# Performance work log

Measured on AMD Instinct MI355X. Metric: run time of the kernel, lower is better.

The kernel has to match this reference:

```python
import jax, jax.numpy as jnp
import numpy as np

B, S, TK, H, E, V, OOV = 16, 8, 400, 256, 128, 50000, 50
H2 = 2 * H


def setup_inputs() -> dict:
    key = jax.random.key(0)
    ks = jax.random.split(key, 24)
    std = 0.02
    d = {}
    d["y_t_1"] = jax.random.randint(ks[0], (B,), 0, V)
    d["h0"] = jax.random.normal(ks[1], (B, H), jnp.float32)
    d["c0"] = jax.random.normal(ks[2], (B, H), jnp.float32)
    d["encoder_output"] = jax.random.normal(ks[3], (B, S, TK, H2), jnp.float32)
    d["section_output"] = jax.random.normal(ks[4], (B, S, H2), jnp.float32)
    d["enc_padding_mask"] = jnp.ones((B, S, TK), jnp.float32)
    d["c_t_1"] = jax.random.normal(ks[5], (B, H2), jnp.float32)
    d["extra_zeros"] = jnp.zeros((B, OOV), jnp.float32)
    d["enc_batch_extend_vocab"] = jax.random.randint(ks[6], (B, S * TK), 0, V + OOV)
    d["coverage"] = jnp.zeros((B, S, TK), jnp.float32)
    d["gamma"] = jnp.ones((B, S, TK), jnp.float32)
    # learned parameters
    d["embedding"] = std * jax.random.normal(ks[7], (V, E), jnp.float32)
    d["W_xc"] = std * jax.random.normal(ks[8], (H2 + E, E), jnp.float32)
    d["b_xc"] = jnp.zeros((E,), jnp.float32)
    d["W_ih"] = std * jax.random.normal(ks[9], (E, 4 * H), jnp.float32)
    d["b_ih"] = jnp.zeros((4 * H,), jnp.float32)
    d["W_hh"] = std * jax.random.normal(ks[10], (H, 4 * H), jnp.float32)
    # pytorch init sets forget-gate bias (2nd quarter) to 1
    d["b_hh"] = jnp.zeros((4 * H,), jnp.float32).at[H:2 * H].set(1.0)
    d["Wh_sec"] = std * jax.random.normal(ks[11], (H2, H2), jnp.float32)
    d["Wd_sec"] = std * jax.random.normal(ks[12], (H2, H2), jnp.float32)
    d["bd_sec"] = jnp.zeros((H2,), jnp.float32)
    d["v_sec"] = std * jax.random.normal(ks[13], (H2, 1), jnp.float32)
    d["Wh_w"] = std * jax.random.normal(ks[14], (H2, H2), jnp.float32)
    d["Wc_w"] = std * jax.random.normal(ks[15], (H2,), jnp.float32)
    d["Wd_w"] = std * jax.random.normal(ks[16], (H2, H2), jnp.float32)
    d["bd_w"] = jnp.zeros((H2,), jnp.float32)
    d["v_w"] = std * jax.random.normal(ks[17], (H2, 1), jnp.float32)
    d["W_pgen"] = std * jax.random.normal(ks[18], (4 * H + E, 1), jnp.float32)
    d["b_pgen"] = jnp.zeros((1,), jnp.float32)
    d["W_out1"] = std * jax.random.normal(ks[19], (3 * H, H), jnp.float32)
    d["b_out1"] = jnp.zeros((H,), jnp.float32)
    d["W_out2"] = std * jax.random.normal(ks[20], (H, V), jnp.float32)
    d["b_out2"] = jnp.zeros((V,), jnp.float32)
    return d


def reference(y_t_1, h0, c0, encoder_output, section_output, enc_padding_mask,
              c_t_1, extra_zeros, enc_batch_extend_vocab, coverage, gamma,
              embedding, W_xc, b_xc, W_ih, b_ih, W_hh, b_hh,
              Wh_sec, Wd_sec, bd_sec, v_sec,
              Wh_w, Wc_w, Wd_w, bd_w, v_w,
              W_pgen, b_pgen, W_out1, b_out1, W_out2, b_out2):
    # embedding + input context projection
    emb = embedding[y_t_1]                                      # [B,E]
    x = jnp.concatenate([c_t_1, emb], axis=1) @ W_xc + b_xc     # [B,E]
    # single-step LSTM (pytorch gate order i,f,g,o)
    gates = x @ W_ih + b_ih + h0 @ W_hh + b_hh                  # [B,4H]
    i, f, g, o = jnp.split(gates, 4, axis=1)
    c = jax.nn.sigmoid(f) * c0 + jax.nn.sigmoid(i) * jnp.tanh(g)
    h = jax.nn.sigmoid(o) * jnp.tanh(c)
    s_t_hat = jnp.concatenate([h, c], axis=1)                   # [B,2H]
    # section attention -> beta [B,S]
    e_sec = jnp.tanh(section_output @ Wh_sec + (s_t_hat @ Wd_sec + bd_sec)[:, None, :])
    sc_sec = jnp.squeeze(e_sec @ v_sec, -1)                     # [B,S]
    beta = jax.nn.softmax(sc_sec, axis=1)
    beta = beta / beta.sum(axis=1, keepdims=True)
    # word attention with coverage feature
    att = encoder_output @ Wh_w + (s_t_hat @ Wd_w + bd_w)[:, None, None, :]
    att = att + coverage[..., None] * Wc_w                      # [B,S,TK,2H]
    sc_w = jnp.squeeze(jnp.tanh(att) @ v_w, -1)                 # [B,S,TK]
    ws = (beta[:, :, None] * sc_w).reshape(B, S * TK)
    mask = enc_padding_mask.reshape(B, S * TK)
    ad = jax.nn.softmax(ws, axis=1) * mask
    attn = ad / ad.sum(axis=1, keepdims=True)                   # [B,S*TK]
    c_t = jnp.einsum('bt,btn->bn', attn, encoder_output.reshape(B, S * TK, H2))
    cov = coverage + attn.reshape(B, S, TK)
    # pointer-gen gate
    p_gen = jax.nn.sigmoid(jnp.concatenate([c_t, s_t_hat, x], axis=1) @ W_pgen + b_pgen)  # [B,1]
    # output vocab distribution
    out = jnp.concatenate([h, c_t], axis=1) @ W_out1 + b_out1
    vocab_dist = jax.nn.softmax(out @ W_out2 + b_out2, axis=1)  # [B,V]
    vd = jnp.concatenate([p_gen * vocab_dist, extra_zeros], axis=1)  # [B,V+OOV]
    ad_ = (1.0 - p_gen) * attn
    rows = jnp.arange(B)[:, None]
    final_dist = vd.at[rows, enc_batch_extend_vocab].add(ad_)
    return (final_dist, h, c, c_t, attn, p_gen, cov)
```

## Files before the change

### kernel.cpp

```cpp
#include <hip/hip_runtime.h>
#include <math.h>

#define BB   16
#define SS   8
#define TKK  400
#define HH   256
#define EE   128
#define VV   50000
#define OOVV 50
#define HH2  512
#define STK  (SS*TKK)
#define VOO  (VV+OOVV)

#define OFF_X     0
#define OFF_ST    2048
#define OFF_SD    10240
#define OFF_WD    18432
#define OFF_SCSEC 26752
#define OFF_SCW   26880
#define OFF_CT    78080
#define OFF_OUT1  86272
#define OFF_PGEN  90368
#define OFF_PSUM  93520
#define OFF_BT    113040

#define O_FD   0
#define O_H    800800
#define O_C    804896
#define O_CT   808992
#define O_ATTN 817184
#define O_PGEN 868384
#define O_COV  868400

#define NLB 391
#define GEMM_NB 800

typedef __attribute__((ext_vector_type(8))) short bf16x8;
typedef __attribute__((ext_vector_type(4))) float f32x4;

__device__ __forceinline__ float sigm(float x){ return 1.0f/(1.0f+expf(-x)); }

__device__ __forceinline__ unsigned short f2b(float f){
  unsigned int u = __float_as_uint(f);
  unsigned int r = (u + 0x7fffu + ((u >> 16) & 1u)) >> 16;
  return (unsigned short)r;
}

__device__ __forceinline__ float tanhfast(float x){
  float cx = fminf(9.0f, fmaxf(-9.0f, x));
  float t = __expf(2.0f*cx);
  return (t - 1.0f) * __builtin_amdgcn_rcpf(t + 1.0f);
}

__device__ __forceinline__ float wave_sum(float v){
  #pragma unroll
  for(int o=32;o>0;o>>=1) v += __shfl_xor(v,o);
  return v;
}
__device__ __forceinline__ float wave_max(float v){
  #pragma unroll
  for(int o=32;o>0;o>>=1) v = fmaxf(v,__shfl_xor(v,o));
  return v;
}

__device__ __forceinline__ void glds16(const void* g, void* l){
  __builtin_amdgcn_global_load_lds((const __attribute__((address_space(1))) void*)g,
                                   (__attribute__((address_space(3))) void*)l, 16, 0, 0);
}

__device__ __forceinline__ bf16x8 cvt8(float4 a, float4 b){
  union{ bf16x8 v; unsigned short u[8]; } t;
  t.u[0]=f2b(a.x); t.u[1]=f2b(a.y); t.u[2]=f2b(a.z); t.u[3]=f2b(a.w);
  t.u[4]=f2b(b.x); t.u[5]=f2b(b.y); t.u[6]=f2b(b.z); t.u[7]=f2b(b.w);
  return t.v;
}

__global__ void k_pre(const float* __restrict__ Whw, unsigned short* __restrict__ Btg,
                      const int* __restrict__ y, const float* __restrict__ ct1,
                      const float* __restrict__ emb, const float* __restrict__ Wxc,
                      const float* __restrict__ bxc, const float* __restrict__ bdsec,
                      const float* __restrict__ bdw, float* __restrict__ ws){
  __shared__ float sm[10440];
  int bi = blockIdx.x, tid = threadIdx.x;
  if(bi < 64){
    int n0 = (bi & 7)*64, k0 = (bi >> 3)*64;
    int tx = tid & 63, ty = tid >> 6;
    #pragma unroll
    for(int it=0; it<16; it++){
      int kk = it*4 + ty;
      sm[kk*65 + tx] = Whw[(size_t)(k0+kk)*HH2 + n0 + tx];
    }
    __syncthreads();
    #pragma unroll
    for(int it=0; it<2; it++){
      int kgl = it*4 + ty;
      int kgG = (k0 >> 3) + kgl;
      int rnd = kgG >> 2, kg = kgG & 3;
      int col = n0 + tx;
      union{ bf16x8 v; unsigned short u[8]; } t;
      #pragma unroll
      for(int j=0;j<8;j++) t.u[j] = f2b(sm[(kgl*8+j)*65 + tx]);
      *(bf16x8*)&Btg[(size_t)rnd*16384 + (size_t)(col*4 + (kg ^ ((col>>1)&3)))*8] = t.v;
    }
  } else if(bi < 80){
    float* cat = sm;
    float* red = sm + 10240;
    for(int f=tid; f<BB*640; f+=256){
      int b = f/640, r = f - b*640;
      cat[f] = (r < HH2) ? ct1[b*HH2 + r] : emb[(size_t)y[b]*EE + (r-HH2)];
    }
    __syncthreads();
    int c = (bi-64)*8 + (tid & 7);
    int b = (tid >> 3) & 15;
    int kh = tid >> 7;
    float acc = 0.0f;
    const float* a = &cat[b*640];
    for(int k=kh*320; k<kh*320+320; k++) acc += a[k]*Wxc[k*EE + c];
    if(kh==1) red[b*8 + (tid&7)] = acc;
    __syncthreads();
    if(kh==0) ws[OFF_X + b*EE + c] = acc + red[b*8 + (tid&7)] + bxc[c];
  } else {
    for(int f=tid; f<BB*HH2; f+=256){
      int c = f & (HH2-1);
      ws[OFF_CT + f] = 0.0f;
      ws[OFF_SD + f] = bdsec[c];
      ws[OFF_WD + f] = bdw[c];
    }
  }
}

__global__ void k_lstm(const float* __restrict__ h0, const float* __restrict__ c0,
                       const float* __restrict__ Wih, const float* __restrict__ bih,
                       const float* __restrict__ Whh, const float* __restrict__ bhh,
                       float* __restrict__ ws, float* __restrict__ out){
  __shared__ float xh[4*384];
  __shared__ float red[3*64*4];
  int tid = threadIdx.x;
  int jc = (blockIdx.x & 15)*16, bc = (blockIdx.x >> 4)*4;
  for(int f=tid; f<4*384; f+=256){
    int bl = f/384, r = f - bl*384;
    xh[f] = (r < EE) ? ws[OFF_X + (bc+bl)*EE + r] : h0[(bc+bl)*HH + (r-EE)];
  }
  __syncthreads();
  int jl = tid & 15, bl = (tid >> 4) & 3, kq = tid >> 6;
  int j = jc + jl, b = bc + bl;
  float a0=0.f, a1=0.f, a2=0.f, a3=0.f;
  const float* a = &xh[bl*384];
  for(int k=kq*96; k<kq*96+96; k++){
    float v = a[k];
    const float* w = (k < EE) ? &Wih[k*4*HH + j] : &Whh[(k-EE)*4*HH + j];
    a0 += v*w[0]; a1 += v*w[HH]; a2 += v*w[2*HH]; a3 += v*w[3*HH];
  }
  if(kq){
    float* r = &red[((kq-1)*64 + bl*16 + jl)*4];
    r[0]=a0; r[1]=a1; r[2]=a2; r[3]=a3;
  }
  __syncthreads();
  if(kq==0){
    #pragma unroll
    for(int p=0;p<3;p++){
      const float* r = &red[(p*64 + bl*16 + jl)*4];
      a0+=r[0]; a1+=r[1]; a2+=r[2]; a3+=r[3];
    }
    a0 += bih[j] + bhh[j];
    a1 += bih[j+HH] + bhh[j+HH];
    a2 += bih[j+2*HH] + bhh[j+2*HH];
    a3 += bih[j+3*HH] + bhh[j+3*HH];
    float c = sigm(a1)*c0[b*HH+j] + sigm(a0)*tanhf(a2);
    float h = sigm(a3)*tanhf(c);
    out[O_H + b*HH + j] = h;
    out[O_C + b*HH + j] = c;
    ws[OFF_ST + b*HH2 + j]      = h;
    ws[OFF_ST + b*HH2 + HH + j] = c;
  }
}

__global__ void k_proj(const float* __restrict__ Wdsec, const float* __restrict__ Wdw,
                       float* __restrict__ ws){
  __shared__ float st[BB*32];
  int tid = threadIdx.x;
  int mi = blockIdx.x >> 5;
  int cb = (blockIdx.x >> 4) & 1;
  int kq = blockIdx.x & 15;
  int k0 = kq*32;
  for(int f=tid; f<BB*32; f+=256){
    int b = f >> 5, kk = f & 31;
    st[f] = ws[OFF_ST + b*HH2 + k0 + kk];
  }
  __syncthreads();
  int c = cb*256 + tid;
  const float* Wm = (mi ? Wdw : Wdsec) + (size_t)k0*HH2 + c;
  float acc[BB];
  #pragma unroll
  for(int b=0;b<BB;b++) acc[b] = 0.0f;
  #pragma unroll 4
  for(int kk=0;kk<32;kk++){
    float wv = Wm[(size_t)kk*HH2];
    #pragma unroll
    for(int b=0;b<BB;b++) acc[b] += st[b*32 + kk]*wv;
  }
  int dst = mi ? OFF_WD : OFF_SD;
  #pragma unroll
  for(int b=0;b<BB;b++) atomicAdd(&ws[dst + b*HH2 + c], acc[b]);
}

__global__ __launch_bounds__(512, 4) void k_gemm6(
        const float* __restrict__ A, const unsigned short* __restrict__ Btg,
        const float* __restrict__ Wcw, const float* __restrict__ vw,
        const float* __restrict__ cover,
        const float* __restrict__ sec, const float* __restrict__ Whsec,
        const float* __restrict__ vsec, float* __restrict__ ws){
  __shared__ __align__(16) unsigned short smem[32768];
  int tid = threadIdx.x;
  if(blockIdx.x >= GEMM_NB){
    float* row = (float*)smem;
    float* red = row + HH2;
    int bi = blockIdx.x - GEMM_NB;
    int b = bi >> 3;
    if(tid < HH2) row[tid] = sec[(size_t)bi*HH2 + tid];
    __syncthreads();
    int col = tid;
    float acc = 0.0f;
    #pragma unroll 8
    for(int k=0;k<HH2;k++) acc += row[k]*Whsec[k*HH2 + col];
    float val = tanhf(acc + ws[OFF_SD + b*HH2 + col]) * vsec[col];
    val = wave_sum(val);
    if((tid&63)==0) red[tid>>6] = val;
    __syncthreads();
    if(tid==0){
      float s = 0.0f;
      #pragma unroll
      for(int i=0;i<8;i++) s += red[i];
      ws[OFF_SCSEC + bi] = s;
    }
    return;
  }
  int w = tid >> 6, lane = tid & 63, m = lane & 15, q = lane >> 4;
  int mk = (m >> 1) & 3, sw = q ^ mk;
  int rg = w >> 2, cg = w & 3;
  int row0 = blockIdx.x * 64;
  int b = blockIdx.x / 50;

  const float* a0p = &A[(size_t)(row0 + rg*32 + m)*HH2 + q*8];
  const float* a1p = a0p + (size_t)16*HH2;

  f32x4 acc0[8], acc1[8];
  #pragma unroll
  for(int j=0;j<8;j++){ acc0[j] = (f32x4){0.f,0.f,0.f,0.f}; acc1[j] = (f32x4){0.f,0.f,0.f,0.f}; }

  float4 pa0, pa1, pa2, pa3;
  bf16x8 af0, af1;

  #define GLDSB(rr, buf) {                                                     \
    const unsigned short* bsrc_ = Btg + (size_t)(rr)*16384;                    \
    unsigned short* ldst_ = &smem[(size_t)(buf)*16384];                        \
    _Pragma("unroll")                                                          \
    for(int i_=0;i_<4;i_++)                                                    \
      glds16(bsrc_ + i_*4096 + tid*8, ldst_ + i_*4096 + tid*8);                \
  }
  #define LOADA(rr) {                                                          \
    pa0 = *(const float4*)(a0p + (rr)*32);                                     \
    pa1 = *(const float4*)(a0p + (rr)*32 + 4);                                 \
    pa2 = *(const float4*)(a1p + (rr)*32);                                     \
    pa3 = *(const float4*)(a1p + (rr)*32 + 4);                                 \
  }

  GLDSB(0, 0);
  LOADA(0);
  GLDSB(1, 1);
  asm volatile("s_waitcnt vmcnt(8)" ::: "memory");
  __builtin_amdgcn_sched_barrier(0);
  af0 = cvt8(pa0, pa1);
  af1 = cvt8(pa2, pa3);
  __builtin_amdgcn_s_barrier();

  for(int r=0; r<16; r++){
    if(r < 15) LOADA(r+1);
    __builtin_amdgcn_s_setprio(1);
    #pragma unroll
    for(int cf=0; cf<8; cf++){
      int col = cg*128 + cf*16 + m;
      bf16x8 bv = *(const bf16x8*)&smem[(size_t)(r&1)*16384 + ((size_t)col*4 + sw)*8];
      acc0[cf] = __builtin_amdgcn_mfma_f32_16x16x32_bf16(af0, bv, acc0[cf], 0,0,0);
      acc1[cf] = __builtin_amdgcn_mfma_f32_16x16x32_bf16(af1, bv, acc1[cf], 0,0,0);
    }
    __builtin_amdgcn_s_setprio(0);
    if(r <= 13){
      asm volatile("s_waitcnt lgkmcnt(0)" ::: "memory");
      __builtin_amdgcn_sched_barrier(0);
      __builtin_amdgcn_s_barrier();
      GLDSB(r+2, r&1);
    }
    if(r < 15){
      if(r <= 13){ asm volatile("s_waitcnt vmcnt(4)" ::: "memory"); }
      else       { asm volatile("s_waitcnt vmcnt(0)" ::: "memory"); }
      __builtin_amdgcn_sched_barrier(0);
      af0 = cvt8(pa0, pa1);
      af1 = cvt8(pa2, pa3);
      __builtin_amdgcn_s_barrier();
    }
  }
  #undef GLDSB
  #undef LOADA

  float cov0[4], cov1[4];
  #pragma unroll
  for(int r=0;r<4;r++){
    cov0[r] = cover[row0 + rg*32 + q*4 + r];
    cov1[r] = cover[row0 + rg*32 + 16 + q*4 + r];
  }
  float rs0[4] = {0,0,0,0}, rs1[4] = {0,0,0,0};
  #pragma unroll
  for(int j=0;j<8;j++){
    int col = cg*128 + j*16 + m;
    float wdv = ws[OFF_WD + b*HH2 + col];
    float wcv = Wcw[col], vwv = vw[col];
    #pragma unroll
    for(int r=0;r<4;r++){
      rs0[r] += tanhfast(acc0[j][r] + wdv + cov0[r]*wcv) * vwv;
      rs1[r] += tanhfast(acc1[j][r] + wdv + cov1[r]*wcv) * vwv;
    }
  }
  __syncthreads();
  float* rbuf = (float*)smem;
  #pragma unroll
  for(int r=0;r<4;r++){
    float v = rs0[r];
    v += __shfl_xor(v,1,16); v += __shfl_xor(v,2,16);
    v += __shfl_xor(v,4,16); v += __shfl_xor(v,8,16);
    if(m==0) rbuf[cg*64 + rg*32 + q*4 + r] = v;
    float u = rs1[r];
    u += __shfl_xor(u,1,16); u += __shfl_xor(u,2,16);
    u += __shfl_xor(u,4,16); u += __shfl_xor(u,8,16);
    if(m==0) rbuf[cg*64 + rg*32 + 16 + q*4 + r] = u;
  }
  __syncthreads();
  if(tid < 64)
    ws[OFF_SCW + row0 + tid] = rbuf[tid] + rbuf[64+tid] + rbuf[128+tid] + rbuf[192+tid];
}

__global__ void k_attn(const float* __restrict__ mask, const float* __restrict__ cover,
                       float* __restrict__ ws, float* __restrict__ out){
  int b = blockIdx.x, tid = threadIdx.x;
  __shared__ float vals[STK];
  __shared__ float redm[16], reds[16];
  __shared__ float sc[SS];
  if(tid < SS) sc[tid] = ws[OFF_SCSEC + b*SS + tid];
  __syncthreads();
  float bm = -1e30f;
  #pragma unroll
  for(int s=0;s<SS;s++) bm = fmaxf(bm, sc[s]);
  float be[SS]; float bsum = 0.0f;
  #pragma unroll
  for(int s=0;s<SS;s++){ be[s] = expf(sc[s]-bm); bsum += be[s]; }
  #pragma unroll
  for(int s=0;s<SS;s++) be[s] /= bsum;
  int lane = tid & 63, w = tid >> 6;
  float m = -1e30f;
  for(int j=tid;j<STK;j+=1024){
    float v = be[j/TKK] * ws[OFF_SCW + b*STK + j];
    vals[j] = v; m = fmaxf(m, v);
  }
  m = wave_max(m);
  if(lane==0) redm[w] = m;
  __syncthreads();
  if(tid < 16){
    float t = redm[tid];
    #pragma unroll
    for(int o=8;o>0;o>>=1) t = fmaxf(t, __shfl_xor(t,o,16));
    if(tid==0) redm[0] = t;
  }
  __syncthreads();
  m = redm[0];
  float ssum = 0.0f;
  for(int j=tid;j<STK;j+=1024){
    float e = expf(vals[j]-m) * mask[b*STK + j];
    vals[j] = e; ssum += e;
  }
  ssum = wave_sum(ssum);
  if(lane==0) reds[w] = ssum;
  __syncthreads();
  if(tid < 16){
    float t = reds[tid];
    #pragma unroll
    for(int o=8;o>0;o>>=1) t += __shfl_xor(t,o,16);
    if(tid==0) reds[0] = t;
  }
  __syncthreads();
  float inv = 1.0f/reds[0];
  for(int j=tid;j<STK;j+=1024){
    float a = vals[j]*inv;
    out[O_ATTN + b*STK + j] = a;
    out[O_COV  + b*STK + j] = cover[b*STK + j] + a;
  }
}

__global__ void k_ct(const float* __restrict__ enc, const float* __restrict__ out,
                     float* __restrict__ ws){
  int b = blockIdx.y, tid = threadIdx.x;
  __shared__ float a[64];
  __shared__ float part[512];
  int t0 = blockIdx.x*64;
  if(tid<64) a[tid] = out[O_ATTN + b*STK + t0 + tid];
  __syncthreads();
  int c4 = tid & 127, rh = tid >> 7;
  const float4* e4 = (const float4*)enc;
  size_t base = ((size_t)(b*STK + t0 + rh*32))*128 + c4;
  float4 acc = {0.f,0.f,0.f,0.f};
  #pragma unroll 8
  for(int rr=0; rr<32; rr++){
    float4 v = e4[base + (size_t)rr*128];
    float av = a[rh*32 + rr];
    acc.x += av*v.x; acc.y += av*v.y; acc.z += av*v.z; acc.w += av*v.w;
  }
  if(rh) *(float4*)&part[c4*4] = acc;
  __syncthreads();
  if(!rh){
    float4 o = *(const float4*)&part[c4*4];
    atomicAdd(&ws[OFF_CT + b*HH2 + c4*4 + 0], acc.x + o.x);
    atomicAdd(&ws[OFF_CT + b*HH2 + c4*4 + 1], acc.y + o.y);
    atomicAdd(&ws[OFF_CT + b*HH2 + c4*4 + 2], acc.z + o.z);
    atomicAdd(&ws[OFF_CT + b*HH2 + c4*4 + 3], acc.w + o.w);
  }
}

__global__ void k_out1(const float* __restrict__ Wp, const float* __restrict__ bp,
                       const float* __restrict__ Wo1, const float* __restrict__ bo1,
                       float* __restrict__ ws, float* __restrict__ out){
  __shared__ float cat[BB*768];
  __shared__ float red[3*64];
  int tid = threadIdx.x;
  if(blockIdx.x == 64){
    int w = tid >> 6, lane = tid & 63;
    #pragma unroll
    for(int i=0;i<4;i++){
      int b = w*4 + i;
      float p = 0.0f;
      for(int k=lane;k<4*HH+EE;k+=64){
        float val = (k < HH2) ? ws[OFF_CT + b*HH2 + k]
                  : (k < 4*HH) ? ws[OFF_ST + b*HH2 + (k-HH2)]
                  : ws[OFF_X + b*EE + (k-4*HH)];
        p += val * Wp[k];
      }
      p = wave_sum(p);
      if(lane==0){
        float pg = sigm(p + bp[0]);
        ws[OFF_PGEN + b] = pg;
        out[O_PGEN + b]  = pg;
      }
    }
    for(int f=tid; f<BB*HH2; f+=256) out[O_CT + f] = ws[OFF_CT + f];
    return;
  }
  for(int f=tid; f<BB*768; f+=256){
    int b = f/768, r = f - b*768;
    cat[f] = (r < HH) ? ws[OFF_ST + b*HH2 + r] : ws[OFF_CT + b*HH2 + (r-HH)];
  }
  __syncthreads();
  int cl = tid & 3, bl = (tid >> 2) & 15, kq = tid >> 6;
  int c = blockIdx.x*4 + cl;
  float acc = 0.0f;
  const float* a = &cat[bl*768];
  for(int k=kq*192; k<kq*192+192; k++) acc += a[k]*Wo1[k*HH + c];
  if(kq) red[(kq-1)*64 + bl*4 + cl] = acc;
  __syncthreads();
  if(kq==0){
    acc += red[bl*4+cl] + red[64 + bl*4+cl] + red[128 + bl*4+cl];
    ws[OFF_OUT1 + bl*HH + c] = acc + bo1[c];
  }
}

__global__ void k_logits(const float* __restrict__ W2, const float* __restrict__ b2,
                         float* __restrict__ ws, float* __restrict__ out){
  int tid = threadIdx.x;
  __shared__ float o1[BB*HH];
  for(int i=tid;i<BB*HH/4;i+=256)
    ((float4*)o1)[i] = ((const float4*)&ws[OFF_OUT1])[i];
  __syncthreads();
  int cl = tid & 31, bq = tid >> 5;
  int c4 = blockIdx.x*128 + cl*4;
  bool ok = c4 < VV;
  int b0 = bq*2, b1 = b0+1;
  float4 acc0 = {0.f,0.f,0.f,0.f}, acc1 = {0.f,0.f,0.f,0.f};
  if(ok){
    const float* oa = &o1[b0*HH];
    const float* ob = &o1[b1*HH];
    #pragma unroll 4
    for(int k=0;k<HH;k++){
      float4 wv = *(const float4*)&W2[(size_t)k*VV + c4];
      float xa = oa[k], xb = ob[k];
      acc0.x += xa*wv.x; acc0.y += xa*wv.y; acc0.z += xa*wv.z; acc0.w += xa*wv.w;
      acc1.x += xb*wv.x; acc1.y += xb*wv.y; acc1.z += xb*wv.z; acc1.w += xb*wv.w;
    }
  }
  float bv[4] = {0,0,0,0};
  if(ok){ float4 t = *(const float4*)&b2[c4]; bv[0]=t.x; bv[1]=t.y; bv[2]=t.z; bv[3]=t.w; }
  float a0[4] = {acc0.x, acc0.y, acc0.z, acc0.w};
  float a1[4] = {acc1.x, acc1.y, acc1.z, acc1.w};
  float s0 = 0.0f, s1 = 0.0f;
  #pragma unroll
  for(int j=0;j<4;j++){
    float e0 = ok ? expf(a0[j]+bv[j]) : 0.0f;
    float e1 = ok ? expf(a1[j]+bv[j]) : 0.0f;
    if(ok){
      out[(size_t)b0*VOO + c4 + j] = e0;
      out[(size_t)b1*VOO + c4 + j] = e1;
    }
    s0 += e0; s1 += e1;
  }
  #pragma unroll
  for(int o=1;o<32;o<<=1){ s0 += __shfl_xor(s0,o,32); s1 += __shfl_xor(s1,o,32); }
  if(cl==0){
    ws[OFF_PSUM + b0*NLB + blockIdx.x] = s0;
    ws[OFF_PSUM + b1*NLB + blockIdx.x] = s1;
  }
}

__global__ void k_final(const float* __restrict__ xz, float* __restrict__ ws,
                        float* __restrict__ out){
  int b = blockIdx.y;
  int v = blockIdx.x*256 + threadIdx.x;
  __shared__ float red[4];
  int lane = threadIdx.x & 63, w = threadIdx.x >> 6;
  float p = 0.0f;
  for(int i=threadIdx.x;i<NLB;i+=256) p += ws[OFF_PSUM + b*NLB + i];
  p = wave_sum(p);
  if(lane==0) red[w] = p;
  __syncthreads();
  float s = red[0]+red[1]+red[2]+red[3];
  float pg = ws[OFF_PGEN + b];
  if(v < VV)       out[(size_t)b*VOO + v] = pg * out[(size_t)b*VOO + v] / s;
  else if(v < VOO) out[(size_t)b*VOO + v] = xz[b*OOVV + (v-VV)];
}

__global__ void k_scatter(const int* __restrict__ ebev, float* __restrict__ ws,
                          float* __restrict__ out){
  int b = blockIdx.y;
  float r = 1.0f - ws[OFF_PGEN + b];
  for(int j=blockIdx.x*256+threadIdx.x;j<STK;j+=1024){
    int idx = ebev[b*STK + j];
    atomicAdd(&out[(size_t)b*VOO + idx], r*out[O_ATTN + b*STK + j]);
  }
}

extern "C" void kernel_launch(void* const* d_in, const int* in_sizes, int n_in,
                              void* d_out, int out_size, void* d_ws, size_t ws_size,
                              hipStream_t stream){
  const int*   y     = (const int*)  d_in[0];
  const float* h0    = (const float*)d_in[1];
  const float* c0    = (const float*)d_in[2];
  const float* enc   = (const float*)d_in[3];
  const float* sec   = (const float*)d_in[4];
  const float* mask  = (const float*)d_in[5];
  const float* ct1   = (const float*)d_in[6];
  const float* xz    = (const float*)d_in[7];
  const int*   ebev  = (const int*)  d_in[8];
  const float* cover = (const float*)d_in[9];
  const float* emb   = (const float*)d_in[11];
  const float* Wxc   = (const float*)d_in[12];
  const float* bxc   = (const float*)d_in[13];
  const float* Wih   = (const float*)d_in[14];
  const float* bih   = (const float*)d_in[15];
  const float* Whh   = (const float*)d_in[16];
  const float* bhh   = (const float*)d_in[17];
  const float* Whsec = (const float*)d_in[18];
  const float* Wdsec = (const float*)d_in[19];
  const float* bdsec = (const float*)d_in[20];
  const float* vsec  = (const float*)d_in[21];
  const float* Whw   = (const float*)d_in[22];
  const float* Wcw   = (const float*)d_in[23];
  const float* Wdw   = (const float*)d_in[24];
  const float* bdw   = (const float*)d_in[25];
  const float* vw    = (const float*)d_in[26];
  const float* Wp    = (const float*)d_in[27];
  const float* bp    = (const float*)d_in[28];
  const float* Wo1   = (const float*)d_in[29];
  const float* bo1   = (const float*)d_in[30];
  const float* Wo2   = (const float*)d_in[31];
  const float* bo2   = (const float*)d_in[32];
  float* out = (float*)d_out;
  float* ws  = (float*)d_ws;
  unsigned short* Btg = (unsigned short*)(ws + OFF_BT);

  k_pre    <<<dim3(81),       dim3(256),  0, stream>>>(Whw, Btg, y, ct1, emb, Wxc, bxc, bdsec, bdw, ws);
  k_lstm   <<<dim3(64),       dim3(256),  0, stream>>>(h0, c0, Wih, bih, Whh, bhh, ws, out);
  k_proj   <<<dim3(64),       dim3(256),  0, stream>>>(Wdsec, Wdw, ws);
  k_gemm6  <<<dim3(928),      dim3(512),  0, stream>>>(enc, Btg, Wcw, vw, cover, sec, Whsec, vsec, ws);
  k_attn   <<<dim3(BB),       dim3(1024), 0, stream>>>(mask, cover, ws, out);
  k_ct     <<<dim3(50,BB),    dim3(256),  0, stream>>>(enc, out, ws);
  k_out1   <<<dim3(65),       dim3(256),  0, stream>>>(Wp, bp, Wo1, bo1, ws, out);
  k_logits <<<dim3(NLB),      dim3(256),  0, stream>>>(Wo2, bo2, ws, out);
  k_final  <<<dim3(196,BB),   dim3(256),  0, stream>>>(xz, ws, out);
  k_scatter<<<dim3(4,BB),     dim3(256),  0, stream>>>(ebev, ws, out);
}
```

Baseline: 475.2 us.

## Load GEMM B tiles directly from global memory instead of staging through LDS

The word-attention GEMM kernel stops staging the bf16 Wh_w tiles into shared memory with global_load_lds double buffering and barriers. Each wave now reads its B fragments straight from global memory, relying on L2/cache reuse, and the swizzle is dropped from the pre-transposed layout. Blocks shrink to 256 threads covering 32 rows, doubling the GEMM grid, and the section-score blocks compute two columns per thread. This removes LDS traffic and block-wide barriers but makes every wave fetch the full B matrix from cache, which raises global/L2 load pressure.

```diff
diff --git a/kernel.cpp b/kernel.cpp
--- a/kernel.cpp
+++ b/kernel.cpp
@@ -33,7 +33,7 @@
 #define O_COV  868400
 
 #define NLB 391
-#define GEMM_NB 800
+#define GEMM_NB 1600
 
 typedef __attribute__((ext_vector_type(8))) short bf16x8;
 typedef __attribute__((ext_vector_type(4))) float f32x4;
@@ -61,11 +61,6 @@
   #pragma unroll
   for(int o=32;o>0;o>>=1) v = fmaxf(v,__shfl_xor(v,o));
   return v;
-}
-
-__device__ __forceinline__ void glds16(const void* g, void* l){
-  __builtin_amdgcn_global_load_lds((const __attribute__((address_space(1))) void*)g,
-                                   (__attribute__((address_space(3))) void*)l, 16, 0, 0);
 }
 
 __device__ __forceinline__ bf16x8 cvt8(float4 a, float4 b){
@@ -100,7 +95,7 @@
       union{ bf16x8 v; unsigned short u[8]; } t;
       #pragma unroll
       for(int j=0;j<8;j++) t.u[j] = f2b(sm[(kgl*8+j)*65 + tx]);
-      *(bf16x8*)&Btg[(size_t)rnd*16384 + (size_t)(col*4 + (kg ^ ((col>>1)&3)))*8] = t.v;
+      *(bf16x8*)&Btg[(size_t)rnd*16384 + (size_t)(col*4 + kg)*8] = t.v;
     }
   } else if(bi < 80){
     float* cat = sm;
@@ -204,110 +199,85 @@
   for(int b=0;b<BB;b++) atomicAdd(&ws[dst + b*HH2 + c], acc[b]);
 }
 
-__global__ __launch_bounds__(512, 4) void k_gemm6(
+__global__ __launch_bounds__(256, 3) void k_gemm6(
         const float* __restrict__ A, const unsigned short* __restrict__ Btg,
         const float* __restrict__ Wcw, const float* __restrict__ vw,
         const float* __restrict__ cover,
         const float* __restrict__ sec, const float* __restrict__ Whsec,
         const float* __restrict__ vsec, float* __restrict__ ws){
-  __shared__ __align__(16) unsigned short smem[32768];
+  __shared__ float sm[520];
   int tid = threadIdx.x;
   if(blockIdx.x >= GEMM_NB){
-    float* row = (float*)smem;
-    float* red = row + HH2;
+    float* row = sm;
+    float* red = sm + 512;
     int bi = blockIdx.x - GEMM_NB;
     int b = bi >> 3;
-    if(tid < HH2) row[tid] = sec[(size_t)bi*HH2 + tid];
+    row[tid]       = sec[(size_t)bi*HH2 + tid];
+    row[tid + 256] = sec[(size_t)bi*HH2 + tid + 256];
     __syncthreads();
-    int col = tid;
-    float acc = 0.0f;
+    float acc0 = 0.0f, acc1 = 0.0f;
     #pragma unroll 8
-    for(int k=0;k<HH2;k++) acc += row[k]*Whsec[k*HH2 + col];
-    float val = tanhf(acc + ws[OFF_SD + b*HH2 + col]) * vsec[col];
+    for(int k=0;k<HH2;k++){
+      float rv = row[k];
+      acc0 += rv*Whsec[(size_t)k*HH2 + tid];
+      acc1 += rv*Whsec[(size_t)k*HH2 + tid + 256];
+    }
+    float val = tanhf(acc0 + ws[OFF_SD + b*HH2 + tid])       * vsec[tid]
+              + tanhf(acc1 + ws[OFF_SD + b*HH2 + tid + 256]) * vsec[tid + 256];
     val = wave_sum(val);
     if((tid&63)==0) red[tid>>6] = val;
     __syncthreads();
-    if(tid==0){
-      float s = 0.0f;
-      #pragma unroll
-      for(int i=0;i<8;i++) s += red[i];
-      ws[OFF_SCSEC + bi] = s;
-    }
+    if(tid==0) ws[OFF_SCSEC + bi] = red[0]+red[1]+red[2]+red[3];
     return;
   }
-  int w = tid >> 6, lane = tid & 63, m = lane & 15, q = lane >> 4;
-  int mk = (m >> 1) & 3, sw = q ^ mk;
-  int rg = w >> 2, cg = w & 3;
-  int row0 = blockIdx.x * 64;
-  int b = blockIdx.x / 50;
-
-  const float* a0p = &A[(size_t)(row0 + rg*32 + m)*HH2 + q*8];
+  int cg = tid >> 6, lane = tid & 63, m = lane & 15, q = lane >> 4;
+  int row0 = blockIdx.x * 32;
+  int b = blockIdx.x / 100;
+
+  const float* a0p = &A[(size_t)(row0 + m)*HH2 + q*8];
   const float* a1p = a0p + (size_t)16*HH2;
+  const unsigned short* bwp = Btg + (size_t)(cg*128 + m)*32 + q*8;
 
   f32x4 acc0[8], acc1[8];
   #pragma unroll
   for(int j=0;j<8;j++){ acc0[j] = (f32x4){0.f,0.f,0.f,0.f}; acc1[j] = (f32x4){0.f,0.f,0.f,0.f}; }
 
-  float4 pa0, pa1, pa2, pa3;
-  bf16x8 af0, af1;
-
-  #define GLDSB(rr, buf) {                                                     \
-    const unsigned short* bsrc_ = Btg + (size_t)(rr)*16384;                    \
-    unsigned short* ldst_ = &smem[(size_t)(buf)*16384];                        \
+  float4 pA0,pA1,pA2,pA3, pB0,pB1,pB2,pB3;
+  #define LOADA(rr, s0,s1,s2,s3) {                       \
+    s0 = *(const float4*)(a0p + (rr)*32);                \
+    s1 = *(const float4*)(a0p + (rr)*32 + 4);            \
+    s2 = *(const float4*)(a1p + (rr)*32);                \
+    s3 = *(const float4*)(a1p + (rr)*32 + 4);            \
+  }
+  #define ROUND(rr, s0,s1,s2,s3) {                                             \
+    bf16x8 af0 = cvt8(s0, s1);                                                 \
+    bf16x8 af1 = cvt8(s2, s3);                                                 \
+    const unsigned short* bp_ = bwp + (size_t)(rr)*16384;                      \
+    bf16x8 bv[8];                                                              \
     _Pragma("unroll")                                                          \
-    for(int i_=0;i_<4;i_++)                                                    \
-      glds16(bsrc_ + i_*4096 + tid*8, ldst_ + i_*4096 + tid*8);                \
-  }
-  #define LOADA(rr) {                                                          \
-    pa0 = *(const float4*)(a0p + (rr)*32);                                     \
-    pa1 = *(const float4*)(a0p + (rr)*32 + 4);                                 \
-    pa2 = *(const float4*)(a1p + (rr)*32);                                     \
-    pa3 = *(const float4*)(a1p + (rr)*32 + 4);                                 \
-  }
-
-  GLDSB(0, 0);
-  LOADA(0);
-  GLDSB(1, 1);
-  asm volatile("s_waitcnt vmcnt(8)" ::: "memory");
-  __builtin_amdgcn_sched_barrier(0);
-  af0 = cvt8(pa0, pa1);
-  af1 = cvt8(pa2, pa3);
-  __builtin_amdgcn_s_barrier();
-
-  for(int r=0; r<16; r++){
-    if(r < 15) LOADA(r+1);
-    __builtin_amdgcn_s_setprio(1);
-    #pragma unroll
-    for(int cf=0; cf<8; cf++){
-      int col = cg*128 + cf*16 + m;
-      bf16x8 bv = *(const bf16x8*)&smem[(size_t)(r&1)*16384 + ((size_t)col*4 + sw)*8];
-      acc0[cf] = __builtin_amdgcn_mfma_f32_16x16x32_bf16(af0, bv, acc0[cf], 0,0,0);
-      acc1[cf] = __builtin_amdgcn_mfma_f32_16x16x32_bf16(af1, bv, acc1[cf], 0,0,0);
-    }
-    __builtin_amdgcn_s_setprio(0);
-    if(r <= 13){
-      asm volatile("s_waitcnt lgkmcnt(0)" ::: "memory");
-      __builtin_amdgcn_sched_barrier(0);
-      __builtin_amdgcn_s_barrier();
-      GLDSB(r+2, r&1);
-    }
-    if(r < 15){
-      if(r <= 13){ asm volatile("s_waitcnt vmcnt(4)" ::: "memory"); }
-      else       { asm volatile("s_waitcnt vmcnt(0)" ::: "memory"); }
-      __builtin_amdgcn_sched_barrier(0);
-      af0 = cvt8(pa0, pa1);
-      af1 = cvt8(pa2, pa3);
-      __builtin_amdgcn_s_barrier();
-    }
-  }
-  #undef GLDSB
+    for(int cf=0;cf<8;cf++) bv[cf] = *(const bf16x8*)(bp_ + cf*512);           \
+    _Pragma("unroll")                                                          \
+    for(int cf=0;cf<8;cf++){                                                   \
+      acc0[cf] = __builtin_amdgcn_mfma_f32_16x16x32_bf16(af0, bv[cf], acc0[cf], 0,0,0); \
+      acc1[cf] = __builtin_amdgcn_mfma_f32_16x16x32_bf16(af1, bv[cf], acc1[cf], 0,0,0); \
+    }                                                                          \
+  }
+
+  LOADA(0, pA0,pA1,pA2,pA3);
+  for(int rp=0; rp<8; rp++){
+    LOADA(2*rp+1, pB0,pB1,pB2,pB3);
+    ROUND(2*rp,   pA0,pA1,pA2,pA3);
+    if(rp < 7) LOADA(2*rp+2, pA0,pA1,pA2,pA3);
+    ROUND(2*rp+1, pB0,pB1,pB2,pB3);
+  }
   #undef LOADA
+  #undef ROUND
 
   float cov0[4], cov1[4];
   #pragma unroll
   for(int r=0;r<4;r++){
-    cov0[r] = cover[row0 + rg*32 + q*4 + r];
-    cov1[r] = cover[row0 + rg*32 + 16 + q*4 + r];
+    cov0[r] = cover[row0 + q*4 + r];
+    cov1[r] = cover[row0 + 16 + q*4 + r];
   }
   float rs0[4] = {0,0,0,0}, rs1[4] = {0,0,0,0};
   #pragma unroll
@@ -321,22 +291,21 @@
       rs1[r] += tanhfast(acc1[j][r] + wdv + cov1[r]*wcv) * vwv;
     }
   }
-  __syncthreads();
-  float* rbuf = (float*)smem;
+  float* rbuf = sm;
   #pragma unroll
   for(int r=0;r<4;r++){
     float v = rs0[r];
     v += __shfl_xor(v,1,16); v += __shfl_xor(v,2,16);
     v += __shfl_xor(v,4,16); v += __shfl_xor(v,8,16);
-    if(m==0) rbuf[cg*64 + rg*32 + q*4 + r] = v;
+    if(m==0) rbuf[cg*32 + q*4 + r] = v;
     float u = rs1[r];
     u += __shfl_xor(u,1,16); u += __shfl_xor(u,2,16);
     u += __shfl_xor(u,4,16); u += __shfl_xor(u,8,16);
-    if(m==0) rbuf[cg*64 + rg*32 + 16 + q*4 + r] = u;
-  }
-  __syncthreads();
-  if(tid < 64)
-    ws[OFF_SCW + row0 + tid] = rbuf[tid] + rbuf[64+tid] + rbuf[128+tid] + rbuf[192+tid];
+    if(m==0) rbuf[cg*32 + 16 + q*4 + r] = u;
+  }
+  __syncthreads();
+  if(tid < 32)
+    ws[OFF_SCW + row0 + tid] = rbuf[tid] + rbuf[32+tid] + rbuf[64+tid] + rbuf[96+tid];
 }
 
 __global__ void k_attn(const float* __restrict__ mask, const float* __restrict__ cover,
@@ -585,7 +554,7 @@
   k_pre    <<<dim3(81),       dim3(256),  0, stream>>>(Whw, Btg, y, ct1, emb, Wxc, bxc, bdsec, bdw, ws);
   k_lstm   <<<dim3(64),       dim3(256),  0, stream>>>(h0, c0, Wih, bih, Whh, bhh, ws, out);
   k_proj   <<<dim3(64),       dim3(256),  0, stream>>>(Wdsec, Wdw, ws);
-  k_gemm6  <<<dim3(928),      dim3(512),  0, stream>>>(enc, Btg, Wcw, vw, cover, sec, Whsec, vsec, ws);
+  k_gemm6  <<<dim3(1728),     dim3(256),  0, stream>>>(enc, Btg, Wcw, vw, cover, sec, Whsec, vsec, ws);
   k_attn   <<<dim3(BB),       dim3(1024), 0, stream>>>(mask, cover, ws, out);
   k_ct     <<<dim3(50,BB),    dim3(256),  0, stream>>>(enc, out, ws);
   k_out1   <<<dim3(65),       dim3(256),  0, stream>>>(Wp, bp, Wo1, bo1, ws, out);
```

After: 504.3 us. +6.1%, slower.

## Split attention GEMM into smaller 256-thread blocks over row and column halves

Applied to the files above, without the earlier changes.

The main encoder-projection GEMM now runs as 32-row tiles split into two column halves per block, with 256 threads and half the LDS, giving four times as many blocks. Because each block now holds only partial word scores, these are combined with atomicAdd into a buffer that is zeroed in the prelude kernel. The section-score tail blocks are adapted to 256 threads, each handling two columns. The aim is better occupancy and load balance on the many-CU GPU, at the cost of reloading each A tile twice, doing twice as many B-tile loads in total, and adding atomics.

```diff
diff --git a/kernel.cpp b/kernel.cpp
--- a/kernel.cpp
+++ b/kernel.cpp
@@ -33,7 +33,7 @@
 #define O_COV  868400
 
 #define NLB 391
-#define GEMM_NB 800
+#define GEMM_NB 3200
 
 typedef __attribute__((ext_vector_type(8))) short bf16x8;
 typedef __attribute__((ext_vector_type(4))) float f32x4;
@@ -126,6 +126,7 @@
       ws[OFF_SD + f] = bdsec[c];
       ws[OFF_WD + f] = bdw[c];
     }
+    for(int f=tid; f<BB*STK; f+=256) ws[OFF_SCW + f] = 0.0f;
   }
 }
 
@@ -204,74 +205,71 @@
   for(int b=0;b<BB;b++) atomicAdd(&ws[dst + b*HH2 + c], acc[b]);
 }
 
-__global__ __launch_bounds__(512, 4) void k_gemm6(
+__global__ __launch_bounds__(256, 4) void k_gemm6(
         const float* __restrict__ A, const unsigned short* __restrict__ Btg,
         const float* __restrict__ Wcw, const float* __restrict__ vw,
         const float* __restrict__ cover,
         const float* __restrict__ sec, const float* __restrict__ Whsec,
         const float* __restrict__ vsec, float* __restrict__ ws){
-  __shared__ __align__(16) unsigned short smem[32768];
+  __shared__ __align__(16) unsigned short smem[16384];
   int tid = threadIdx.x;
   if(blockIdx.x >= GEMM_NB){
     float* row = (float*)smem;
     float* red = row + HH2;
     int bi = blockIdx.x - GEMM_NB;
     int b = bi >> 3;
-    if(tid < HH2) row[tid] = sec[(size_t)bi*HH2 + tid];
+    row[tid]       = sec[(size_t)bi*HH2 + tid];
+    row[tid + 256] = sec[(size_t)bi*HH2 + tid + 256];
     __syncthreads();
-    int col = tid;
-    float acc = 0.0f;
+    float acc0 = 0.0f, acc1 = 0.0f;
     #pragma unroll 8
-    for(int k=0;k<HH2;k++) acc += row[k]*Whsec[k*HH2 + col];
-    float val = tanhf(acc + ws[OFF_SD + b*HH2 + col]) * vsec[col];
+    for(int k=0;k<HH2;k++){
+      float rv = row[k];
+      acc0 += rv*Whsec[(size_t)k*HH2 + tid];
+      acc1 += rv*Whsec[(size_t)k*HH2 + tid + 256];
+    }
+    float val = tanhf(acc0 + ws[OFF_SD + b*HH2 + tid])       * vsec[tid]
+              + tanhf(acc1 + ws[OFF_SD + b*HH2 + tid + 256]) * vsec[tid + 256];
     val = wave_sum(val);
     if((tid&63)==0) red[tid>>6] = val;
     __syncthreads();
-    if(tid==0){
-      float s = 0.0f;
-      #pragma unroll
-      for(int i=0;i<8;i++) s += red[i];
-      ws[OFF_SCSEC + bi] = s;
-    }
+    if(tid==0) ws[OFF_SCSEC + bi] = red[0]+red[1]+red[2]+red[3];
     return;
   }
   int w = tid >> 6, lane = tid & 63, m = lane & 15, q = lane >> 4;
   int mk = (m >> 1) & 3, sw = q ^ mk;
-  int rg = w >> 2, cg = w & 3;
-  int row0 = blockIdx.x * 64;
-  int b = blockIdx.x / 50;
-
-  const float* a0p = &A[(size_t)(row0 + rg*32 + m)*HH2 + q*8];
-  const float* a1p = a0p + (size_t)16*HH2;
-
-  f32x4 acc0[8], acc1[8];
-  #pragma unroll
-  for(int j=0;j<8;j++){ acc0[j] = (f32x4){0.f,0.f,0.f,0.f}; acc1[j] = (f32x4){0.f,0.f,0.f,0.f}; }
-
-  float4 pa0, pa1, pa2, pa3;
-  bf16x8 af0, af1;
+  int rg = w >> 1, cg = w & 1;
+  int rt = blockIdx.x >> 1, ch = blockIdx.x & 1;
+  int row0 = rt * 32;
+  int b = rt / 100;
+
+  const float* a0p = &A[(size_t)(row0 + rg*16 + m)*HH2 + q*8];
+
+  f32x4 acc[8];
+  #pragma unroll
+  for(int j=0;j<8;j++) acc[j] = (f32x4){0.f,0.f,0.f,0.f};
+
+  float4 pa0, pa1;
+  bf16x8 af;
 
   #define GLDSB(rr, buf) {                                                     \
-    const unsigned short* bsrc_ = Btg + (size_t)(rr)*16384;                    \
-    unsigned short* ldst_ = &smem[(size_t)(buf)*16384];                        \
+    const unsigned short* bsrc_ = Btg + (size_t)(rr)*16384 + (size_t)ch*8192;  \
+    unsigned short* ldst_ = &smem[(size_t)(buf)*8192];                         \
     _Pragma("unroll")                                                          \
     for(int i_=0;i_<4;i_++)                                                    \
-      glds16(bsrc_ + i_*4096 + tid*8, ldst_ + i_*4096 + tid*8);                \
+      glds16(bsrc_ + i_*2048 + tid*8, ldst_ + i_*2048 + tid*8);                \
   }
   #define LOADA(rr) {                                                          \
     pa0 = *(const float4*)(a0p + (rr)*32);                                     \
     pa1 = *(const float4*)(a0p + (rr)*32 + 4);                                 \
-    pa2 = *(const float4*)(a1p + (rr)*32);                                     \
-    pa3 = *(const float4*)(a1p + (rr)*32 + 4);                                 \
   }
 
   GLDSB(0, 0);
   LOADA(0);
   GLDSB(1, 1);
-  asm volatile("s_waitcnt vmcnt(8)" ::: "memory");
+  asm volatile("s_waitcnt vmcnt(6)" ::: "memory");
   __builtin_amdgcn_sched_barrier(0);
-  af0 = cvt8(pa0, pa1);
-  af1 = cvt8(pa2, pa3);
+  af = cvt8(pa0, pa1);
   __builtin_amdgcn_s_barrier();
 
   for(int r=0; r<16; r++){
@@ -279,10 +277,9 @@
     __builtin_amdgcn_s_setprio(1);
     #pragma unroll
     for(int cf=0; cf<8; cf++){
-      int col = cg*128 + cf*16 + m;
-      bf16x8 bv = *(const bf16x8*)&smem[(size_t)(r&1)*16384 + ((size_t)col*4 + sw)*8];
-      acc0[cf] = __builtin_amdgcn_mfma_f32_16x16x32_bf16(af0, bv, acc0[cf], 0,0,0);
-      acc1[cf] = __builtin_amdgcn_mfma_f32_16x16x32_bf16(af1, bv, acc1[cf], 0,0,0);
+      int lcol = cg*128 + cf*16 + m;
+      bf16x8 bv = *(const bf16x8*)&smem[(size_t)(r&1)*8192 + ((size_t)lcol*4 + sw)*8];
+      acc[cf] = __builtin_amdgcn_mfma_f32_16x16x32_bf16(af, bv, acc[cf], 0,0,0);
     }
     __builtin_amdgcn_s_setprio(0);
     if(r <= 13){
@@ -292,51 +289,41 @@
       GLDSB(r+2, r&1);
     }
     if(r < 15){
-      if(r <= 13){ asm volatile("s_waitcnt vmcnt(4)" ::: "memory"); }
-      else       { asm volatile("s_waitcnt vmcnt(0)" ::: "memory"); }
+      if(r <= 13){ asm volatile("s_waitcnt vmcnt(6)" ::: "memory"); }
+      else       { asm volatile("s_waitcnt vmcnt(2)" ::: "memory"); }
       __builtin_amdgcn_sched_barrier(0);
-      af0 = cvt8(pa0, pa1);
-      af1 = cvt8(pa2, pa3);
+      af = cvt8(pa0, pa1);
       __builtin_amdgcn_s_barrier();
     }
   }
   #undef GLDSB
   #undef LOADA
 
-  float cov0[4], cov1[4];
-  #pragma unroll
-  for(int r=0;r<4;r++){
-    cov0[r] = cover[row0 + rg*32 + q*4 + r];
-    cov1[r] = cover[row0 + rg*32 + 16 + q*4 + r];
-  }
-  float rs0[4] = {0,0,0,0}, rs1[4] = {0,0,0,0};
+  float cov[4];
+  #pragma unroll
+  for(int r=0;r<4;r++) cov[r] = cover[row0 + rg*16 + q*4 + r];
+  float rsum[4] = {0,0,0,0};
   #pragma unroll
   for(int j=0;j<8;j++){
-    int col = cg*128 + j*16 + m;
+    int col = ch*256 + cg*128 + j*16 + m;
     float wdv = ws[OFF_WD + b*HH2 + col];
     float wcv = Wcw[col], vwv = vw[col];
     #pragma unroll
-    for(int r=0;r<4;r++){
-      rs0[r] += tanhfast(acc0[j][r] + wdv + cov0[r]*wcv) * vwv;
-      rs1[r] += tanhfast(acc1[j][r] + wdv + cov1[r]*wcv) * vwv;
-    }
+    for(int r=0;r<4;r++)
+      rsum[r] += tanhfast(acc[j][r] + wdv + cov[r]*wcv) * vwv;
   }
   __syncthreads();
   float* rbuf = (float*)smem;
   #pragma unroll
   for(int r=0;r<4;r++){
-    float v = rs0[r];
+    float v = rsum[r];
     v += __shfl_xor(v,1,16); v += __shfl_xor(v,2,16);
     v += __shfl_xor(v,4,16); v += __shfl_xor(v,8,16);
-    if(m==0) rbuf[cg*64 + rg*32 + q*4 + r] = v;
-    float u = rs1[r];
-    u += __shfl_xor(u,1,16); u += __shfl_xor(u,2,16);
-    u += __shfl_xor(u,4,16); u += __shfl_xor(u,8,16);
-    if(m==0) rbuf[cg*64 + rg*32 + 16 + q*4 + r] = u;
-  }
-  __syncthreads();
-  if(tid < 64)
-    ws[OFF_SCW + row0 + tid] = rbuf[tid] + rbuf[64+tid] + rbuf[128+tid] + rbuf[192+tid];
+    if(m==0) rbuf[cg*32 + rg*16 + q*4 + r] = v;
+  }
+  __syncthreads();
+  if(tid < 32)
+    atomicAdd(&ws[OFF_SCW + row0 + tid], rbuf[tid] + rbuf[32 + tid]);
 }
 
 __global__ void k_attn(const float* __restrict__ mask, const float* __restrict__ cover,
@@ -585,7 +572,7 @@
   k_pre    <<<dim3(81),       dim3(256),  0, stream>>>(Whw, Btg, y, ct1, emb, Wxc, bxc, bdsec, bdw, ws);
   k_lstm   <<<dim3(64),       dim3(256),  0, stream>>>(h0, c0, Wih, bih, Whh, bhh, ws, out);
   k_proj   <<<dim3(64),       dim3(256),  0, stream>>>(Wdsec, Wdw, ws);
-  k_gemm6  <<<dim3(928),      dim3(512),  0, stream>>>(enc, Btg, Wcw, vw, cover, sec, Whsec, vsec, ws);
+  k_gemm6  <<<dim3(3328),     dim3(256),  0, stream>>>(enc, Btg, Wcw, vw, cover, sec, Whsec, vsec, ws);
   k_attn   <<<dim3(BB),       dim3(1024), 0, stream>>>(mask, cover, ws, out);
   k_ct     <<<dim3(50,BB),    dim3(256),  0, stream>>>(enc, out, ws);
   k_out1   <<<dim3(65),       dim3(256),  0, stream>>>(Wp, bp, Wo1, bo1, ws, out);
```

Result: slower. 497.5 us (+4.7%).
